# Performance work log

Measured on AMD Instinct MI355X. Metric: run time of the kernel, lower is better.

Reference implementation:

```python
import jax, jax.numpy as jnp
import numpy as np

B, T, W, L, H, TW = 2, 4096, 2048, 2048, 8, 4
HD = L // H  # head dim for block-diagonal gate projections


def setup_inputs() -> dict:
    key = jax.random.key(0)
    ks = jax.random.split(key, 16)
    inv_sqrt_w = 1.0 / np.sqrt(W)
    inv_sqrt_l = 1.0 / np.sqrt(L)
    inv_sqrt_hd = 1.0 / np.sqrt(HD)
    return {
        "x": jax.random.normal(ks[0], (B, T, W), dtype=jnp.float32),
        "segment_pos": jnp.tile(jnp.arange(T, dtype=jnp.int32), (B, 1)),
        # linear_y, linear_x: width -> lru_width
        "w_y": jax.random.normal(ks[1], (W, L), dtype=jnp.float32) * inv_sqrt_w,
        "b_y": jnp.zeros((L,), dtype=jnp.float32),
        "w_x": jax.random.normal(ks[2], (W, L), dtype=jnp.float32) * inv_sqrt_w,
        "b_x": jnp.zeros((L,), dtype=jnp.float32),
        # linear_out: lru_width -> width
        "w_out": jax.random.normal(ks[3], (L, W), dtype=jnp.float32) * inv_sqrt_l,
        "b_out": jnp.zeros((W,), dtype=jnp.float32),
        # depthwise causal temporal conv, kernel [TW, L]
        "conv_w": jax.random.normal(ks[4], (TW, L), dtype=jnp.float32) / np.sqrt(TW),
        "conv_b": jnp.zeros((L,), dtype=jnp.float32),
        # RG-LRU: a_param and two block-diagonal gate projections
        "a_param": jax.random.uniform(ks[5], (L,), dtype=jnp.float32, minval=-2.0, maxval=1.0),
        "igate_w": jax.random.normal(ks[6], (H, HD, HD), dtype=jnp.float32) * inv_sqrt_hd,
        "igate_b": jnp.zeros((H, HD), dtype=jnp.float32),
        "agate_w": jax.random.normal(ks[7], (H, HD, HD), dtype=jnp.float32) * inv_sqrt_hd,
        "agate_b": jnp.zeros((H, HD), dtype=jnp.float32),
    }


def _block_diag_linear(u, w, b):
    # u: [B,T,L] -> [B,T,H,HD] blockwise projected -> [B,T,L]
    uh = u.reshape(u.shape[0], u.shape[1], H, HD)
    y = jnp.einsum("bthd,hde->bthe", uh, w) + b
    return y.reshape(u.shape)


def _forward(x, segment_pos, w_y, b_y, w_x, b_x, w_out, b_out,
             conv_w, conv_b, a_param, igate_w, igate_b, agate_w, agate_b):
    # gate branch: linear_y + tanh-approx GELU
    y = jax.nn.gelu(jnp.einsum("btw,wl->btl", x, w_y) + b_y, approximate=True)
    # recurrent branch: linear_x
    xb = jnp.einsum("btw,wl->btl", x, w_x) + b_x
    # causal depthwise temporal conv (width TW), zero history before t=0
    x_pad = jnp.pad(xb, ((0, 0), (TW - 1, 0), (0, 0)))
    conv = conv_b + sum(conv_w[j] * x_pad[:, j:j + T] for j in range(TW))
    # RG-LRU gates
    gate_x = jax.nn.sigmoid(_block_diag_linear(conv, igate_w, igate_b))
    gate_a = jax.nn.sigmoid(_block_diag_linear(conv, agate_w, agate_b))
    log_a = -8.0 * gate_a * jax.nn.softplus(a_param)  # [B,T,L]
    a = jnp.exp(log_a)
    reset = (segment_pos == 0)[..., None]  # [B,T,1]
    multiplier = jnp.sqrt(1.0 - jnp.exp(2.0 * log_a))
    multiplier = jnp.where(reset, 1.0, multiplier)
    normed = conv * gate_x * multiplier
    a_masked = jnp.where(reset, 0.0, a)
    # diagonal linear recurrence: h_t = a_t * h_{t-1} + normed_t
    def step(h, inp):
        a_t, x_t = inp
        h = a_t * h + x_t
        return h, h
    h0 = jnp.zeros((x.shape[0], L), dtype=x.dtype)
    _, hs = jax.lax.scan(step, h0, (a_masked.transpose(1, 0, 2), normed.transpose(1, 0, 2)))
    hs = hs.transpose(1, 0, 2)  # [B,T,L]
    # elementwise gate then output projection
    return jnp.einsum("btl,lw->btw", hs * y, w_out) + b_out


def reference(x, segment_pos, w_y, b_y, w_x, b_x, w_out, b_out,
              conv_w, conv_b, a_param, igate_w, igate_b, agate_w, agate_b):
    return _forward(x, segment_pos, w_y, b_y, w_x, b_x, w_out, b_out,
                    conv_w, conv_b, a_param, igate_w, igate_b, agate_w, agate_b)
```

## Files before the change

kernel.cpp:

```cpp
#include <hip/hip_runtime.h>
#include <cstdint>
#include <math.h>

typedef _Float16 f16;
typedef f16 f16x8 __attribute__((ext_vector_type(8)));
typedef f16 f16x4 __attribute__((ext_vector_type(4)));
typedef float f32x4 __attribute__((ext_vector_type(4)));

#define BATCH 2
#define TSEQ 4096
#define WID 2048
#define LRU 2048
#define NHEAD 8
#define HDIM 256
#define MTOT (BATCH * TSEQ)
#define CT 128
#define NC (TSEQ / CT)

__device__ __forceinline__ void gl2lds16(const f16* g, f16* l) {
  __builtin_amdgcn_global_load_lds(
      (__attribute__((address_space(1))) uint32_t*)(uintptr_t)g,
      (__attribute__((address_space(3))) uint32_t*)(uint32_t)(uintptr_t)l,
      16, 0, 0);
}

__device__ __forceinline__ float fast_rcp(float x) {
  float r; asm("v_rcp_f32 %0, %1" : "=v"(r) : "v"(x)); return r;
}
__device__ __forceinline__ float fast_sigmoid(float x) {
  return fast_rcp(1.f + __expf(-x));
}
__device__ __forceinline__ float f16bits_to_f(uint32_t b) {
  return (float)__builtin_bit_cast(f16, (uint16_t)b);
}

__global__ void prep_kernel(const float* __restrict__ x, f16* __restrict__ Xh,
                            const float* __restrict__ w_y, const float* __restrict__ w_x,
                            const float* __restrict__ w_out,
                            f16* __restrict__ wyT, f16* __restrict__ wxT, f16* __restrict__ woutT,
                            const float* __restrict__ ig, const float* __restrict__ ag,
                            f16* __restrict__ igT, f16* __restrict__ agT,
                            const float* __restrict__ ap, float* __restrict__ spT) {
  __shared__ float tile[32][33];
  const int bid = blockIdx.x, t = threadIdx.x;
  if (bid < 16384) {
    int i = bid * 256 + t;
    float4 v = ((const float4*)x)[i];
    f16x4 o = { (f16)v.x, (f16)v.y, (f16)v.z, (f16)v.w };
    ((f16x4*)Xh)[i] = o;
    return;
  }
  if (bid >= 29696) {
    int i = (bid - 29696) * 256 + t;
    spT[i] = log1pf(expf(ap[i]));
    return;
  }
  const int tx = t & 31, ty = t >> 5;
  const float* ib; f16* ob; int R, C, c0, r0;
  if (bid < 28672) {
    int idx = bid - 16384;
    int z = idx >> 12, tl = idx & 4095;
    ib = z == 0 ? w_y : (z == 1 ? w_x : w_out);
    ob = z == 0 ? wyT : (z == 1 ? wxT : woutT);
    R = 2048; C = 2048;
    c0 = (tl & 63) * 32; r0 = (tl >> 6) * 32;
  } else {
    int idx = bid - 28672;
    int z = idx >> 6, tl = idx & 63;
    ib = (z < 8 ? ig : ag) + (long long)(z & 7) * HDIM * HDIM;
    ob = (z < 8 ? igT : agT) + (long long)(z & 7) * HDIM * HDIM;
    R = HDIM; C = HDIM;
    c0 = (tl & 7) * 32; r0 = (tl >> 3) * 32;
  }
#pragma unroll
  for (int i = 0; i < 32; i += 8)
    tile[ty + i][tx] = ib[(long long)(r0 + ty + i) * C + c0 + tx];
  __syncthreads();
#pragma unroll
  for (int i = 0; i < 32; i += 8)
    ob[(long long)(c0 + ty + i) * R + r0 + tx] = (f16)tile[tx][ty + i];
}

template <int MODE>
__global__ __launch_bounds__(512, 2) void gemm_256(
    const f16* __restrict__ A, const f16* __restrict__ BT,
    const float* __restrict__ bias, void* __restrict__ Cout,
    int M, int N, int K) {
  __shared__ __align__(16) f16 As[3][256 * 32];
  __shared__ __align__(16) f16 Bs[3][256 * 32];
  const int m0 = blockIdx.x * 256, n0 = blockIdx.y * 256;
  const int t = threadIdx.x;
  const int lane = t & 63, wave = t >> 6;
  const int wr = (wave >> 2) * 128;
  const int wc = (wave & 3) * 64;
  const int l15 = lane & 15, quad = lane >> 4;
  const int srow = t >> 2;
  const int sg = ((t & 3) ^ ((srow >> 1) & 3)) * 8;
  const int sl = (quad ^ ((l15 >> 1) & 3)) * 8;

  const f16* Ag = A + (long long)(m0 + srow) * K + sg;
  const f16* Bg = BT + (long long)(n0 + srow) * K + sg;
  const long long h128 = (long long)128 * K;

  auto STAGE_A = [&](int tt, int bb) {
    const f16* a = Ag + tt * 32;
    gl2lds16(a, &As[bb][t * 8]);
    gl2lds16(a + h128, &As[bb][128 * 32 + t * 8]);
  };
  auto STAGE_B = [&](int tt, int bb) {
    const f16* b = Bg + tt * 32;
    gl2lds16(b, &Bs[bb][t * 8]);
    gl2lds16(b + h128, &Bs[bb][128 * 32 + t * 8]);
  };

  f32x4 c[8][4] = {};
  const int NT = K >> 5;
  STAGE_A(0, 0); STAGE_B(0, 0); STAGE_A(1, 1); STAGE_B(1, 1);
  asm volatile("s_waitcnt vmcnt(4)" ::: "memory");
  __builtin_amdgcn_s_barrier();
  __builtin_amdgcn_sched_barrier(0);
  int bufc = 0, bufs = 2;
  for (int tt = 0; tt < NT; ++tt) {
    const f16* asrc = &As[bufc][0];
    const f16* bsrc = &Bs[bufc][0];
    f16x8 af[8], bf[4];
#pragma unroll
    for (int i = 0; i < 4; ++i)
      af[i] = *(const f16x8*)&asrc[(wr + i * 16 + l15) * 32 + sl];
#pragma unroll
    for (int j = 0; j < 4; ++j)
      bf[j] = *(const f16x8*)&bsrc[(wc + j * 16 + l15) * 32 + sl];
    if (tt + 2 < NT) STAGE_A(tt + 2, bufs);
    __builtin_amdgcn_s_barrier();
    asm volatile("s_waitcnt lgkmcnt(0)" ::: "memory");
    __builtin_amdgcn_sched_barrier(0);
    __builtin_amdgcn_s_setprio(1);
#pragma unroll
    for (int i = 0; i < 4; ++i)
#pragma unroll
      for (int j = 0; j < 4; ++j)
        c[i][j] = __builtin_amdgcn_mfma_f32_16x16x32_f16(af[i], bf[j], c[i][j], 0, 0, 0);
    __builtin_amdgcn_s_setprio(0);
    __builtin_amdgcn_s_barrier();
#pragma unroll
    for (int i = 4; i < 8; ++i)
      af[i] = *(const f16x8*)&asrc[(wr + i * 16 + l15) * 32 + sl];
    if (tt + 2 < NT) STAGE_B(tt + 2, bufs);
    if (tt + 1 < NT) {
      if (tt + 2 < NT) { asm volatile("s_waitcnt vmcnt(4)" ::: "memory"); }
      else             { asm volatile("s_waitcnt vmcnt(0)" ::: "memory"); }
    }
    __builtin_amdgcn_s_barrier();
    asm volatile("s_waitcnt lgkmcnt(0)" ::: "memory");
    __builtin_amdgcn_sched_barrier(0);
    __builtin_amdgcn_s_setprio(1);
#pragma unroll
    for (int i = 4; i < 8; ++i)
#pragma unroll
      for (int j = 0; j < 4; ++j)
        c[i][j] = __builtin_amdgcn_mfma_f32_16x16x32_f16(af[i], bf[j], c[i][j], 0, 0, 0);
    __builtin_amdgcn_s_setprio(0);
    __builtin_amdgcn_s_barrier();
    bufc = (bufc + 1 == 3) ? 0 : bufc + 1;
    bufs = (bufs + 1 == 3) ? 0 : bufs + 1;
  }
#pragma unroll
  for (int i = 0; i < 8; ++i) {
#pragma unroll
    for (int j = 0; j < 4; ++j) {
      const int col = n0 + wc + j * 16 + l15;
      const float bv = bias[col];
      const int row0 = m0 + wr + i * 16 + quad * 4;
#pragma unroll
      for (int r = 0; r < 4; ++r) {
        float v = c[i][j][r] + bv;
        long long off = (long long)(row0 + r) * N + col;
        if constexpr (MODE == 0) {
          float u = v + 0.044715f * v * v * v;
          float g = 0.5f * v * (1.f + tanhf(0.7978845608028654f * u));
          ((f16*)Cout)[off] = (f16)g;
        } else if constexpr (MODE == 1) {
          ((f16*)Cout)[off] = (f16)v;
        } else {
          ((float*)Cout)[off] = v;
        }
      }
    }
  }
}

__global__ __launch_bounds__(256, 2) void gates_fused(
    const f16* __restrict__ XBh, const float* __restrict__ cw, const float* __restrict__ cb,
    const f16* __restrict__ BiT, const f16* __restrict__ BaT,
    const float* __restrict__ ib, const float* __restrict__ ab,
    const float* __restrict__ spT, const int* __restrict__ segpos,
    uint32_t* __restrict__ AN, float* __restrict__ Ac, float* __restrict__ Hc) {
  __shared__ __align__(16) f16 As[128 * 256];
  __shared__ __align__(16) f16 Bi[128 * 32];
  __shared__ __align__(16) f16 Ba[128 * 32];
  const int m0 = blockIdx.x * 128;
  const int h = blockIdx.y >> 1;
  const int half = blockIdx.y & 1;
  const int ncol0 = h * HDIM + half * 128;
  const int t = threadIdx.x;
  const int lane = t & 63, wave = t >> 6;
  const int wr = (wave >> 1) * 64, wc = (wave & 1) * 64;
  const int l15 = lane & 15, quad = lane >> 4;

#pragma unroll 4
  for (int it = 0; it < 16; ++it) {
    int idx = it * 256 + t;
    int r = idx >> 5, kc = idx & 31;
    int m = m0 + r, tpos = m & (TSEQ - 1);
    int colbase = h * HDIM + kc * 8;
    float acc[8];
    {
      float4 c0 = *(const float4*)&cb[colbase];
      float4 c1 = *(const float4*)&cb[colbase + 4];
      acc[0] = c0.x; acc[1] = c0.y; acc[2] = c0.z; acc[3] = c0.w;
      acc[4] = c1.x; acc[5] = c1.y; acc[6] = c1.z; acc[7] = c1.w;
    }
#pragma unroll
    for (int d = 0; d < 4; ++d) {
      if (tpos >= d) {
        f16x8 xv = *(const f16x8*)&XBh[(long long)(m - d) * LRU + colbase];
        float4 w0 = *(const float4*)&cw[(3 - d) * LRU + colbase];
        float4 w1 = *(const float4*)&cw[(3 - d) * LRU + colbase + 4];
        acc[0] += w0.x * (float)xv[0]; acc[1] += w0.y * (float)xv[1];
        acc[2] += w0.z * (float)xv[2]; acc[3] += w0.w * (float)xv[3];
        acc[4] += w1.x * (float)xv[4]; acc[5] += w1.y * (float)xv[5];
        acc[6] += w1.z * (float)xv[6]; acc[7] += w1.w * (float)xv[7];
      }
    }
    f16x8 o;
#pragma unroll
    for (int k = 0; k < 8; ++k) o[k] = (f16)acc[k];
    int gs = (kc & ~7) | ((kc ^ r) & 7);
    *(f16x8*)&As[r * 256 + gs * 8] = o;
  }
  __syncthreads();

  const int srow = t >> 2, scol = (t & 3) * 8;
  const f16* Big = BiT + (long long)(ncol0 + srow) * HDIM + scol;
  const f16* Bag = BaT + (long long)(ncol0 + srow) * HDIM + scol;
  f32x4 ci[4][4] = {};
  f32x4 ca[4][4] = {};
  for (int k0 = 0; k0 < HDIM; k0 += 32) {
    gl2lds16(Big, &Bi[t * 8]); gl2lds16(Big + 64 * HDIM, &Bi[64 * 32 + t * 8]);
    gl2lds16(Bag, &Ba[t * 8]); gl2lds16(Bag + 64 * HDIM, &Ba[64 * 32 + t * 8]);
    Big += 32; Bag += 32;
    __syncthreads();
    f16x8 af[4], bif[4], baf[4];
#pragma unroll
    for (int i = 0; i < 4; ++i) {
      int row = wr + i * 16 + l15;
      int g = (k0 >> 3) + quad;
      int gsw = (g & ~7) | ((g ^ row) & 7);
      af[i] = *(const f16x8*)&As[row * 256 + gsw * 8];
    }
#pragma unroll
    for (int j = 0; j < 4; ++j) {
      bif[j] = *(const f16x8*)&Bi[(wc + j * 16 + l15) * 32 + quad * 8];
      baf[j] = *(const f16x8*)&Ba[(wc + j * 16 + l15) * 32 + quad * 8];
    }
#pragma unroll
    for (int i = 0; i < 4; ++i)
#pragma unroll
      for (int j = 0; j < 4; ++j) {
        ci[i][j] = __builtin_amdgcn_mfma_f32_16x16x32_f16(af[i], bif[j], ci[i][j], 0, 0, 0);
        ca[i][j] = __builtin_amdgcn_mfma_f32_16x16x32_f16(af[i], baf[j], ca[i][j], 0, 0, 0);
      }
    __syncthreads();
  }

  const int mb = m0 >> 12;
  const int cch = (m0 & (TSEQ - 1)) >> 7;
  uint32_t rsmask = 0;
#pragma unroll
  for (int i = 0; i < 4; ++i) {
    int4 sp4 = *(const int4*)&segpos[m0 + wr + i * 16 + quad * 4];
    rsmask |= (sp4.x == 0 ? 1u : 0u) << (i * 4 + 0);
    rsmask |= (sp4.y == 0 ? 1u : 0u) << (i * 4 + 1);
    rsmask |= (sp4.z == 0 ? 1u : 0u) << (i * 4 + 2);
    rsmask |= (sp4.w == 0 ? 1u : 0u) << (i * 4 + 3);
  }
  float Aw[4], hw[4];
#pragma unroll
  for (int j = 0; j < 4; ++j) {
    const int cl = wc + j * 16 + l15;
    const int col = ncol0 + cl;
    const float ibv = ib[col], abv = ab[col];
    const float sp = spT[col];
    float A4[4], h4[4];
#pragma unroll
    for (int i = 0; i < 4; ++i) {
      float Aseg = 1.f, hseg = 0.f;
#pragma unroll
      for (int r = 0; r < 4; ++r) {
        const int rowL = wr + i * 16 + quad * 4 + r;
        const int row = m0 + rowL;
        float gx = fast_sigmoid(ci[i][j][r] + ibv);
        float ga = fast_sigmoid(ca[i][j][r] + abv);
        float la = -8.f * ga * sp;
        bool rs = (rsmask >> (i * 4 + r)) & 1u;
        float a = rs ? 0.f : __expf(la);
        uint32_t afx = __float2uint_rn(a * 65536.f);
        if (afx > 65535u) afx = 65535u;
        float aq = (float)afx * (1.f / 65536.f);
        int cfull = half * 128 + cl;
        int g = cfull >> 3, e = cfull & 7;
        int gsw = (g & ~7) | ((g ^ rowL) & 7);
        float cv = (float)As[rowL * 256 + gsw * 8 + e];
        float mult = rs ? 1.f : sqrtf(fmaxf(1.f - aq * aq, 0.f));
        f16 nh = (f16)(cv * gx * mult);
        AN[(long long)row * LRU + col] =
            afx | ((uint32_t)__builtin_bit_cast(uint16_t, nh) << 16);
        float xq = (float)nh;
        hseg = aq * hseg + xq;
        Aseg *= aq;
      }
      A4[i] = Aseg; h4[i] = hseg;
    }
#pragma unroll
    for (int i = 0; i < 4; ++i) {
      float A = A4[i], hv = h4[i];
#pragma unroll
      for (int d = 1; d <= 2; d <<= 1) {
        int src = quad >= d ? lane - 16 * d : lane;
        float Ap = __shfl(A, src);
        float hp = __shfl(hv, src);
        if (quad >= d) { hv = A * hp + hv; A = Ap * A; }
      }
      A4[i] = __shfl(A, 48 + l15);
      h4[i] = __shfl(hv, 48 + l15);
    }
    float Awv = 1.f, hwv = 0.f;
#pragma unroll
    for (int i = 0; i < 4; ++i) { hwv = A4[i] * hwv + h4[i]; Awv *= A4[i]; }
    Aw[j] = Awv; hw[j] = hwv;
  }
  float* carry = (float*)Bi;
  __syncthreads();
  if (wr == 0 && quad == 0) {
#pragma unroll
    for (int j = 0; j < 4; ++j) {
      int cl = wc + j * 16 + l15;
      carry[cl * 2] = Aw[j]; carry[cl * 2 + 1] = hw[j];
    }
  }
  __syncthreads();
  if (wr == 64 && quad == 0) {
#pragma unroll
    for (int j = 0; j < 4; ++j) {
      int cl = wc + j * 16 + l15;
      float At = carry[cl * 2], ht = carry[cl * 2 + 1];
      float A = At * Aw[j];
      float hv = Aw[j] * ht + hw[j];
      int o = (mb * NC + cch) * LRU + ncol0 + cl;
      Ac[o] = A; Hc[o] = hv;
    }
  }
}

__global__ void scan23_kernel(const uint32_t* __restrict__ AN,
                              const float* __restrict__ Ac, const float* __restrict__ Hc,
                              const f16* __restrict__ Yh, f16* __restrict__ G) {
  int l = blockIdx.x * 256 + threadIdx.x;
  int c = blockIdx.y, b = blockIdx.z;
  float hv = 0.f;
  for (int cc = 0; cc < c; ++cc) {
    int o = (b * NC + cc) * LRU + l;
    hv = Ac[o] * hv + Hc[o];
  }
  long long base = ((long long)b * TSEQ + (long long)c * CT) * LRU + l;
#pragma unroll 4
  for (int s = 0; s < CT; ++s) {
    long long o = base + (long long)s * LRU;
    uint32_t p = AN[o];
    float a = (float)(p & 0xFFFFu) * (1.f / 65536.f);
    float x = f16bits_to_f(p >> 16);
    hv = a * hv + x;
    G[o] = (f16)(hv * (float)Yh[o]);
  }
}

extern "C" void kernel_launch(void* const* d_in, const int* in_sizes, int n_in,
                              void* d_out, int out_size, void* d_ws, size_t ws_size,
                              hipStream_t stream) {
  (void)in_sizes; (void)n_in; (void)out_size; (void)ws_size;
  const float* x          = (const float*)d_in[0];
  const int*   segment_pos= (const int*)d_in[1];
  const float* w_y        = (const float*)d_in[2];
  const float* b_y        = (const float*)d_in[3];
  const float* w_x        = (const float*)d_in[4];
  const float* b_x        = (const float*)d_in[5];
  const float* w_out      = (const float*)d_in[6];
  const float* b_out      = (const float*)d_in[7];
  const float* conv_w     = (const float*)d_in[8];
  const float* conv_b     = (const float*)d_in[9];
  const float* a_param    = (const float*)d_in[10];
  const float* igate_w    = (const float*)d_in[11];
  const float* igate_b    = (const float*)d_in[12];
  const float* agate_w    = (const float*)d_in[13];
  const float* agate_b    = (const float*)d_in[14];
  float* out = (float*)d_out;

  char* base = (char*)d_ws;
  size_t off = 0;
  auto alloc = [&](size_t nbytes) -> void* {
    void* p = base + off;
    off = (off + nbytes + 255) & ~(size_t)255;
    return p;
  };
  f16*     Xh    = (f16*)alloc((size_t)MTOT * LRU * 2);
  f16*     Yh    = (f16*)alloc((size_t)MTOT * LRU * 2);
  f16*     XBh   = (f16*)alloc((size_t)MTOT * LRU * 2);
  uint32_t* AN   = (uint32_t*)alloc((size_t)MTOT * LRU * 4);
  f16*     wyT   = (f16*)alloc((size_t)WID * LRU * 2);
  f16*     wxT   = (f16*)alloc((size_t)WID * LRU * 2);
  f16*     woutT = (f16*)alloc((size_t)LRU * WID * 2);
  f16*     igwT  = (f16*)alloc((size_t)NHEAD * HDIM * HDIM * 2);
  f16*     agwT  = (f16*)alloc((size_t)NHEAD * HDIM * HDIM * 2);
  float*   Ac    = (float*)alloc((size_t)BATCH * NC * LRU * 4);
  float*   Hc    = (float*)alloc((size_t)BATCH * NC * LRU * 4);
  float*   spT   = (float*)alloc((size_t)LRU * 4);
  f16*     G     = Xh;

  prep_kernel<<<29704, 256, 0, stream>>>(x, Xh, w_y, w_x, w_out, wyT, wxT, woutT,
                                         igate_w, agate_w, igwT, agwT, a_param, spT);
  gemm_256<0><<<dim3(MTOT / 256, LRU / 256), 512, 0, stream>>>(
      Xh, wyT, b_y, Yh, MTOT, LRU, WID);
  gemm_256<1><<<dim3(MTOT / 256, LRU / 256), 512, 0, stream>>>(
      Xh, wxT, b_x, XBh, MTOT, LRU, WID);
  gates_fused<<<dim3(MTOT / 128, 2 * NHEAD), 256, 0, stream>>>(
      XBh, conv_w, conv_b, igwT, agwT, igate_b, agate_b, spT, segment_pos, AN, Ac, Hc);
  scan23_kernel<<<dim3(LRU / 256, NC, BATCH), 256, 0, stream>>>(AN, Ac, Hc, Yh, G);
  gemm_256<2><<<dim3(MTOT / 256, WID / 256), 512, 0, stream>>>(
      G, woutT, b_out, out, MTOT, WID, LRU);
}
```

Baseline: 531.4 us.

## Process full head per gates block to avoid duplicate conv, prefetch weights earlier

The gates kernel now uses 512 threads and covers a whole 256-column head per block instead of splitting each head into two 128-column halves. The depthwise conv tile (128x256) is therefore computed once per head rather than twice, removing redundant XBh loads and conv arithmetic. The first gate-weight slice load is issued before the conv phase so it can overlap with it, and later slices load after each MMA step. The tradeoff is fewer, larger blocks with more LDS per block (64KB A plus 32KB B), which may cut occupancy.

```diff
diff --git a/kernel.cpp b/kernel.cpp
--- a/kernel.cpp
+++ b/kernel.cpp
@@ -189,30 +189,38 @@
   }
 }
 
-__global__ __launch_bounds__(256, 2) void gates_fused(
+__global__ __launch_bounds__(512, 2) void gates_fused(
     const f16* __restrict__ XBh, const float* __restrict__ cw, const float* __restrict__ cb,
     const f16* __restrict__ BiT, const f16* __restrict__ BaT,
     const float* __restrict__ ib, const float* __restrict__ ab,
     const float* __restrict__ spT, const int* __restrict__ segpos,
     uint32_t* __restrict__ AN, float* __restrict__ Ac, float* __restrict__ Hc) {
   __shared__ __align__(16) f16 As[128 * 256];
-  __shared__ __align__(16) f16 Bi[128 * 32];
-  __shared__ __align__(16) f16 Ba[128 * 32];
+  __shared__ __align__(16) f16 Bi[256 * 32];
+  __shared__ __align__(16) f16 Ba[256 * 32];
   const int m0 = blockIdx.x * 128;
-  const int h = blockIdx.y >> 1;
-  const int half = blockIdx.y & 1;
-  const int ncol0 = h * HDIM + half * 128;
+  const int h = blockIdx.y;
+  const int ncol0 = h * HDIM;
   const int t = threadIdx.x;
   const int lane = t & 63, wave = t >> 6;
-  const int wr = (wave >> 1) * 64, wc = (wave & 1) * 64;
+  const int wr = (wave >> 2) * 64;
+  const int wc = (wave & 3) * 64;
   const int l15 = lane & 15, quad = lane >> 4;
 
+  const int srow = t >> 2, scol = (t & 3) * 8;
+  const f16* Big = BiT + (long long)(ncol0 + srow) * HDIM + scol;
+  const f16* Bag = BaT + (long long)(ncol0 + srow) * HDIM + scol;
+  gl2lds16(Big, &Bi[t * 8]);
+  gl2lds16(Big + (long long)128 * HDIM, &Bi[128 * 32 + t * 8]);
+  gl2lds16(Bag, &Ba[t * 8]);
+  gl2lds16(Bag + (long long)128 * HDIM, &Ba[128 * 32 + t * 8]);
+
 #pragma unroll 4
-  for (int it = 0; it < 16; ++it) {
-    int idx = it * 256 + t;
+  for (int it = 0; it < 8; ++it) {
+    int idx = it * 512 + t;
     int r = idx >> 5, kc = idx & 31;
     int m = m0 + r, tpos = m & (TSEQ - 1);
-    int colbase = h * HDIM + kc * 8;
+    int colbase = ncol0 + kc * 8;
     float acc[8];
     {
       float4 c0 = *(const float4*)&cb[colbase];
@@ -240,16 +248,9 @@
   }
   __syncthreads();
 
-  const int srow = t >> 2, scol = (t & 3) * 8;
-  const f16* Big = BiT + (long long)(ncol0 + srow) * HDIM + scol;
-  const f16* Bag = BaT + (long long)(ncol0 + srow) * HDIM + scol;
   f32x4 ci[4][4] = {};
   f32x4 ca[4][4] = {};
   for (int k0 = 0; k0 < HDIM; k0 += 32) {
-    gl2lds16(Big, &Bi[t * 8]); gl2lds16(Big + 64 * HDIM, &Bi[64 * 32 + t * 8]);
-    gl2lds16(Bag, &Ba[t * 8]); gl2lds16(Bag + 64 * HDIM, &Ba[64 * 32 + t * 8]);
-    Big += 32; Bag += 32;
-    __syncthreads();
     f16x8 af[4], bif[4], baf[4];
 #pragma unroll
     for (int i = 0; i < 4; ++i) {
@@ -271,6 +272,15 @@
         ca[i][j] = __builtin_amdgcn_mfma_f32_16x16x32_f16(af[i], baf[j], ca[i][j], 0, 0, 0);
       }
     __syncthreads();
+    if (k0 + 32 < HDIM) {
+      const f16* bi2 = Big + (k0 + 32);
+      const f16* ba2 = Bag + (k0 + 32);
+      gl2lds16(bi2, &Bi[t * 8]);
+      gl2lds16(bi2 + (long long)128 * HDIM, &Bi[128 * 32 + t * 8]);
+      gl2lds16(ba2, &Ba[t * 8]);
+      gl2lds16(ba2 + (long long)128 * HDIM, &Ba[128 * 32 + t * 8]);
+      __syncthreads();
+    }
   }
 
   const int mb = m0 >> 12;
@@ -307,8 +317,7 @@
         uint32_t afx = __float2uint_rn(a * 65536.f);
         if (afx > 65535u) afx = 65535u;
         float aq = (float)afx * (1.f / 65536.f);
-        int cfull = half * 128 + cl;
-        int g = cfull >> 3, e = cfull & 7;
+        int g = cl >> 3, e = cl & 7;
         int gsw = (g & ~7) | ((g ^ rowL) & 7);
         float cv = (float)As[rowL * 256 + gsw * 8 + e];
         float mult = rs ? 1.f : sqrtf(fmaxf(1.f - aq * aq, 0.f));
@@ -432,7 +441,7 @@
       Xh, wyT, b_y, Yh, MTOT, LRU, WID);
   gemm_256<1><<<dim3(MTOT / 256, LRU / 256), 512, 0, stream>>>(
       Xh, wxT, b_x, XBh, MTOT, LRU, WID);
-  gates_fused<<<dim3(MTOT / 128, 2 * NHEAD), 256, 0, stream>>>(
+  gates_fused<<<dim3(MTOT / 128, NHEAD), 512, 0, stream>>>(
       XBh, conv_w, conv_b, igwT, agwT, igate_b, agate_b, spT, segment_pos, AN, Ac, Hc);
   scan23_kernel<<<dim3(LRU / 256, NC, BATCH), 256, 0, stream>>>(AN, Ac, Hc, Yh, G);
   gemm_256<2><<<dim3(MTOT / 256, WID / 256), 512, 0, stream>>>(
```

Result: faster. 519.1 us (-2.3%).
